# Optimization experiments

Hardware: AMD Instinct MI355X
Metric: run time of the kernel (lower is better)

## Reference

```python
import jax, jax.numpy as jnp
import numpy as np

B, N = 128, 2048
QUERY_DIM, NODE_DIM, OUT_DIM = 256, 128, 256
LAMBDA_INIT = 0.8
LN_EPS = 1e-5


def setup_inputs() -> dict:
    key = jax.random.key(0)
    ks = jax.random.split(key, 8)
    fp_vec = jax.random.normal(ks[0], (B, QUERY_DIM), dtype=jnp.float32)
    node_mat = jax.random.normal(ks[1], (B, N, NODE_DIM), dtype=jnp.float32)
    mask = jax.random.uniform(ks[2], (B, N)) < 0.75
    s = 1.0 / np.sqrt(QUERY_DIM)
    Wq1 = jax.random.uniform(ks[3], (NODE_DIM, QUERY_DIM), minval=-s, maxval=s, dtype=jnp.float32)
    Wq2 = jax.random.uniform(ks[4], (NODE_DIM, QUERY_DIM), minval=-s, maxval=s, dtype=jnp.float32)
    s2 = 1.0 / np.sqrt(NODE_DIM)
    Wk = jax.random.uniform(ks[5], (NODE_DIM, NODE_DIM), minval=-s2, maxval=s2, dtype=jnp.float32)
    Wv = jax.random.uniform(ks[6], (OUT_DIM, NODE_DIM), minval=-s2, maxval=s2, dtype=jnp.float32)
    lambda_logit = jnp.zeros((1,), dtype=jnp.float32)
    gamma = jnp.ones((OUT_DIM,), dtype=jnp.float32)
    beta = jnp.zeros((OUT_DIM,), dtype=jnp.float32)
    return {"fp_vec": fp_vec, "node_mat": node_mat, "mask": mask,
            "Wq1": Wq1, "Wq2": Wq2, "Wk": Wk, "Wv": Wv,
            "lambda_logit": lambda_logit, "gamma": gamma, "beta": beta}


def reference(fp_vec, node_mat, mask, Wq1, Wq2, Wk, Wv, lambda_logit, gamma, beta):
    node_dim = node_mat.shape[-1]
    inv_scale = 1.0 / jnp.sqrt(jnp.asarray(node_dim, jnp.float32))
    # projections (torch Linear: y = x @ W.T)
    q1 = fp_vec @ Wq1.T            # (B, node_dim)
    q2 = fp_vec @ Wq2.T            # (B, node_dim)
    k = jnp.einsum('bnd,ed->bne', node_mat, Wk)   # (B, N, node_dim)
    v = jnp.einsum('bnd,od->bno', node_mat, Wv)   # (B, N, out_dim)
    # single-query scores over nodes
    s1 = jnp.einsum('bd,bnd->bn', q1, k) * inv_scale
    s2 = jnp.einsum('bd,bnd->bn', q2, k) * inv_scale
    pad = jnp.where(mask, 0.0, -1e9).astype(s1.dtype)  # (B, N)
    A1 = jax.nn.softmax(s1 + pad, axis=-1)
    A2 = jax.nn.softmax(s2 + pad, axis=-1)
    lam = LAMBDA_INIT + jax.nn.sigmoid(lambda_logit) * 0.2  # (1,)
    A_diff = A1 - lam * A2         # dropout inactive (eval)
    z = jnp.einsum('bn,bno->bo', A_diff, v)  # (B, out_dim)
    # LayerNorm
    mu = jnp.mean(z, axis=-1, keepdims=True)
    var = jnp.mean(jnp.square(z - mu), axis=-1, keepdims=True)
    return (z - mu) * jax.lax.rsqrt(var + LN_EPS) * gamma + beta
```

## Files before the change

kernel.cpp:

```cpp
#include <hip/hip_runtime.h>
#include <hip/hip_bf16.h>
#include <math.h>

#define BB 128
#define NN 2048
#define ND 128
#define QD 256
#define OD 256

#define NPART 8
#define ROWS_PER_BLOCK (NN / NPART)
#define ROWS_PER_WAVE  (ROWS_PER_BLOCK / 4)
#define STEPS 8
#define STEP_ROWS (ROWS_PER_WAVE / STEPS)
#define STEP_BYTES (STEP_ROWS * ND * 4)
#define PART_STRIDE 260

#define EXP2F(x) __builtin_amdgcn_exp2f(x)

typedef __attribute__((address_space(1))) const void gvoid_t;
typedef __attribute__((address_space(3))) void lvoid_t;

__global__ __launch_bounds__(128) void proj_kernel(
    const float* __restrict__ fp_vec, const float* __restrict__ Wq1,
    const float* __restrict__ Wq2, const float* __restrict__ Wk,
    float* __restrict__ qk1g, float* __restrict__ qk2g)
{
  __shared__ __align__(16) float fp_s[QD];
  __shared__ float q1_s[ND];
  __shared__ float q2_s[ND];
  const int b = blockIdx.x, t = threadIdx.x;
  fp_s[t]       = fp_vec[b * QD + t];
  fp_s[t + 128] = fp_vec[b * QD + 128 + t];
  __syncthreads();
  float a1 = 0.f, a2 = 0.f;
  const float4* w1p = (const float4*)(Wq1 + t * QD);
  const float4* w2p = (const float4*)(Wq2 + t * QD);
  #pragma unroll 8
  for (int q = 0; q < QD / 4; ++q) {
    float4 wa = w1p[q], wb = w2p[q];
    float4 f = *(const float4*)&fp_s[q * 4];
    a1 += f.x * wa.x + f.y * wa.y + f.z * wa.z + f.w * wa.w;
    a2 += f.x * wb.x + f.y * wb.y + f.z * wb.z + f.w * wb.w;
  }
  q1_s[t] = a1;
  q2_s[t] = a2;
  __syncthreads();
  float k1 = 0.f, k2 = 0.f;
  #pragma unroll 8
  for (int e = 0; e < ND; ++e) {
    float wv = Wk[e * ND + t];
    k1 += q1_s[e] * wv;
    k2 += q2_s[e] * wv;
  }
  const float cscale = 0.08838834764831845f * 1.4426950408889634f;
  qk1g[b * ND + t] = k1 * cscale;
  qk2g[b * ND + t] = k2 * cscale;
}

__global__ __launch_bounds__(256, 4) void attn_kernel(
    const float* __restrict__ node, const int* __restrict__ mask,
    const float* __restrict__ qk1g, const float* __restrict__ qk2g,
    float* __restrict__ part)
{
  const int bid = blockIdx.x;
  const int b   = bid >> 3;
  const int oct = bid & (NPART - 1);
  const int t = threadIdx.x;
  const int w = t >> 6;
  const int lane = t & 63;
  const int half = lane >> 5;
  const int hl = lane & 31;

  __shared__ __align__(16) float tile_s[4][2][STEP_ROWS * ND];
  __shared__ __align__(16) float sw1[4][ND], sw2[4][ND];
  __shared__ float sl1[4], sl2[4];

  const int wrow0 = oct * ROWS_PER_BLOCK + w * ROWS_PER_WAVE;

  const float4 qk1 = *(const float4*)(qk1g + b * ND + hl * 4);
  const float4 qk2 = *(const float4*)(qk2g + b * ND + hl * 4);
  const int mv = mask[b * NN + wrow0 + lane];

  const char* gbase = (const char*)node + (size_t)(b * NN + wrow0) * (ND * 4);
  char* lb0 = (char*)&tile_s[w][0][0];
  char* lb1 = (char*)&tile_s[w][1][0];

  #pragma unroll
  for (int i = 0; i < 4; ++i)
    __builtin_amdgcn_global_load_lds(
        (gvoid_t*)(gbase + lane * 16 + i * 1024),
        (lvoid_t*)(lb0 + i * 1024), 16, 0, 0);
  #pragma unroll
  for (int i = 0; i < 4; ++i)
    __builtin_amdgcn_global_load_lds(
        (gvoid_t*)(gbase + STEP_BYTES + lane * 16 + i * 1024),
        (lvoid_t*)(lb1 + i * 1024), 16, 0, 0);

  const float pv = mv ? 0.f : -1e9f;

  float l1 = 0.f, l2 = 0.f;
  float4 w1 = make_float4(0.f, 0.f, 0.f, 0.f);
  float4 w2 = make_float4(0.f, 0.f, 0.f, 0.f);

  #pragma unroll 2
  for (int s = 0; s < STEPS; ++s) {
    if (s < STEPS - 1) asm volatile("s_waitcnt vmcnt(4)" ::: "memory");
    else               asm volatile("s_waitcnt vmcnt(0)" ::: "memory");
    __builtin_amdgcn_sched_barrier(0);

    const float* buf = &tile_s[w][s & 1][0];
    const int ib = s * STEP_ROWS;

    #pragma unroll
    for (int j = 0; j < STEP_ROWS / 2; ++j) {
      const float4 x = *(const float4*)&buf[(2 * j + half) * ND + hl * 4];
      float d1 = x.x * qk1.x + x.y * qk1.y + x.z * qk1.z + x.w * qk1.w;
      float d2 = x.x * qk2.x + x.y * qk2.y + x.z * qk2.z + x.w * qk2.w;
      float e1 = d1 + __shfl_xor(d1, 1, 64);
      float e2 = d2 + __shfl_xor(d2, 1, 64);
      float m = (lane & 1) ? e2 : e1;
      m += __shfl_xor(m, 2, 64);
      m += __shfl_xor(m, 4, 64);
      m += __shfl_xor(m, 8, 64);
      m += __shfl_xor(m, 16, 64);
      const float mo = __shfl_xor(m, 1, 64);
      const float s1 = (lane & 1) ? mo : m;
      const float s2 = (lane & 1) ? m : mo;
      const float pad = __shfl(pv, ib + 2 * j + half, 64);
      const float p1 = EXP2F(s1 + pad);
      const float p2 = EXP2F(s2 + pad);
      l1 += p1;
      l2 += p2;
      w1.x += p1 * x.x; w1.y += p1 * x.y; w1.z += p1 * x.z; w1.w += p1 * x.w;
      w2.x += p2 * x.x; w2.y += p2 * x.y; w2.z += p2 * x.z; w2.w += p2 * x.w;
    }

    asm volatile("s_waitcnt lgkmcnt(0)" ::: "memory");
    if (s + 2 < STEPS) {
      const char* gs = gbase + (size_t)(s + 2) * STEP_BYTES + lane * 16;
      char* ls = (char*)&tile_s[w][s & 1][0];
      #pragma unroll
      for (int i = 0; i < 4; ++i)
        __builtin_amdgcn_global_load_lds(
            (gvoid_t*)(gs + i * 1024),
            (lvoid_t*)(ls + i * 1024), 16, 0, 0);
    }
  }

  l1 += __shfl_xor(l1, 32, 64);
  l2 += __shfl_xor(l2, 32, 64);
  w1.x += __shfl_xor(w1.x, 32, 64); w1.y += __shfl_xor(w1.y, 32, 64);
  w1.z += __shfl_xor(w1.z, 32, 64); w1.w += __shfl_xor(w1.w, 32, 64);
  w2.x += __shfl_xor(w2.x, 32, 64); w2.y += __shfl_xor(w2.y, 32, 64);
  w2.z += __shfl_xor(w2.z, 32, 64); w2.w += __shfl_xor(w2.w, 32, 64);
  if (half == 0) {
    *(float4*)&sw1[w][hl * 4] = w1;
    *(float4*)&sw2[w][hl * 4] = w2;
    if (hl == 0) { sl1[w] = l1; sl2[w] = l2; }
  }
  __syncthreads();

  float* po = part + (size_t)bid * PART_STRIDE;
  if (t == 0) {
    po[0] = sl1[0] + sl1[1] + sl1[2] + sl1[3];
    po[1] = sl2[0] + sl2[1] + sl2[2] + sl2[3];
  }
  if (t < ND) {
    po[4 + t]   = sw1[0][t] + sw1[1][t] + sw1[2][t] + sw1[3][t];
    po[132 + t] = sw2[0][t] + sw2[1][t] + sw2[2][t] + sw2[3][t];
  }
}

__global__ __launch_bounds__(256) void finish_kernel(
    const float* __restrict__ part, const float* __restrict__ Wv,
    const float* __restrict__ lambda_logit, const float* __restrict__ gamma,
    const float* __restrict__ beta, float* __restrict__ out)
{
  const int b = blockIdx.x, t = threadIdx.x;
  __shared__ __align__(16) float wd_s[ND];
  __shared__ float red[8];

  const float lam = 0.8f + 0.2f / (1.f + __expf(-lambda_logit[0]));
  const float* pb = part + (size_t)b * NPART * PART_STRIDE;

  if (t < ND) {
    float L1 = 0.f, L2 = 0.f, W1 = 0.f, W2 = 0.f;
    #pragma unroll
    for (int i = 0; i < NPART; ++i) {
      const float* pc = pb + (size_t)i * PART_STRIDE;
      L1 += pc[0];
      L2 += pc[1];
      W1 += pc[4 + t];
      W2 += pc[132 + t];
    }
    wd_s[t] = W1 / L1 - lam * (W2 / L2);
  }
  __syncthreads();

  float z = 0.f;
  const float4* wvp = (const float4*)(Wv + t * ND);
  #pragma unroll 8
  for (int d = 0; d < ND / 4; ++d) {
    const float4 w = wvp[d];
    const float4 f = *(const float4*)&wd_s[d * 4];
    z += f.x * w.x + f.y * w.y + f.z * w.z + f.w * w.w;
  }

  const int wave = t >> 6, lane = t & 63;
  float s = z;
  #pragma unroll
  for (int off = 32; off; off >>= 1) s += __shfl_xor(s, off, 64);
  if (lane == 0) red[wave] = s;
  __syncthreads();
  const float mu = (red[0] + red[1] + red[2] + red[3]) * (1.f / OD);
  const float dz = z - mu;
  float vs = dz * dz;
  #pragma unroll
  for (int off = 32; off; off >>= 1) vs += __shfl_xor(vs, off, 64);
  if (lane == 0) red[wave + 4] = vs;
  __syncthreads();
  const float var = (red[4] + red[5] + red[6] + red[7]) * (1.f / OD);
  out[b * OD + t] = dz * rsqrtf(var + 1e-5f) * gamma[t] + beta[t];
}

extern "C" void kernel_launch(void* const* d_in, const int* in_sizes, int n_in,
                              void* d_out, int out_size, void* d_ws, size_t ws_size,
                              hipStream_t stream) {
  const float* fp_vec = (const float*)d_in[0];
  const float* node   = (const float*)d_in[1];
  const int*   mask   = (const int*)d_in[2];
  const float* Wq1    = (const float*)d_in[3];
  const float* Wq2    = (const float*)d_in[4];
  const float* Wk     = (const float*)d_in[5];
  const float* Wv     = (const float*)d_in[6];
  const float* ll     = (const float*)d_in[7];
  const float* gamma  = (const float*)d_in[8];
  const float* beta   = (const float*)d_in[9];
  float* out = (float*)d_out;

  float* qk1g = (float*)d_ws;
  float* qk2g = qk1g + BB * ND;
  float* part = qk2g + BB * ND;

  proj_kernel<<<BB, 128, 0, stream>>>(fp_vec, Wq1, Wq2, Wk, qk1g, qk2g);
  attn_kernel<<<BB * NPART, 256, 0, stream>>>(node, mask, qk1g, qk2g, part);
  finish_kernel<<<BB, 256, 0, stream>>>(part, Wv, ll, gamma, beta, out);
}
```

Baseline: 235.7 us.

## Replace LDS double-buffered async loads with direct global loads and more partitions

Removes the per-wave LDS staging pipeline built on global_load_lds with manual vmcnt waits, and has each lane read its float4 node slice straight from global memory in a loop unrolled by 4. The partition count per batch doubles to 16, so there are twice as many blocks, each with 32 rows per wave. The aim is to drop LDS traffic and waitcnt stalls and raise occupancy and parallelism, relying on the compiler's unrolling to keep enough loads in flight. In exchange, latency hiding is no longer explicit, and the finish kernel must reduce twice as many partials.

```diff
diff --git a/kernel.cpp b/kernel.cpp
--- a/kernel.cpp
+++ b/kernel.cpp
@@ -8,18 +8,12 @@
 #define QD 256
 #define OD 256
 
-#define NPART 8
+#define NPART 16
 #define ROWS_PER_BLOCK (NN / NPART)
 #define ROWS_PER_WAVE  (ROWS_PER_BLOCK / 4)
-#define STEPS 8
-#define STEP_ROWS (ROWS_PER_WAVE / STEPS)
-#define STEP_BYTES (STEP_ROWS * ND * 4)
 #define PART_STRIDE 260
 
 #define EXP2F(x) __builtin_amdgcn_exp2f(x)
-
-typedef __attribute__((address_space(1))) const void gvoid_t;
-typedef __attribute__((address_space(3))) void lvoid_t;
 
 __global__ __launch_bounds__(128) void proj_kernel(
     const float* __restrict__ fp_vec, const float* __restrict__ Wq1,
@@ -64,7 +58,7 @@
     float* __restrict__ part)
 {
   const int bid = blockIdx.x;
-  const int b   = bid >> 3;
+  const int b   = bid >> 4;
   const int oct = bid & (NPART - 1);
   const int t = threadIdx.x;
   const int w = t >> 6;
@@ -72,7 +66,6 @@
   const int half = lane >> 5;
   const int hl = lane & 31;
 
-  __shared__ __align__(16) float tile_s[4][2][STEP_ROWS * ND];
   __shared__ __align__(16) float sw1[4][ND], sw2[4][ND];
   __shared__ float sl1[4], sl2[4];
 
@@ -80,72 +73,37 @@
 
   const float4 qk1 = *(const float4*)(qk1g + b * ND + hl * 4);
   const float4 qk2 = *(const float4*)(qk2g + b * ND + hl * 4);
-  const int mv = mask[b * NN + wrow0 + lane];
-
-  const char* gbase = (const char*)node + (size_t)(b * NN + wrow0) * (ND * 4);
-  char* lb0 = (char*)&tile_s[w][0][0];
-  char* lb1 = (char*)&tile_s[w][1][0];
-
-  #pragma unroll
-  for (int i = 0; i < 4; ++i)
-    __builtin_amdgcn_global_load_lds(
-        (gvoid_t*)(gbase + lane * 16 + i * 1024),
-        (lvoid_t*)(lb0 + i * 1024), 16, 0, 0);
-  #pragma unroll
-  for (int i = 0; i < 4; ++i)
-    __builtin_amdgcn_global_load_lds(
-        (gvoid_t*)(gbase + STEP_BYTES + lane * 16 + i * 1024),
-        (lvoid_t*)(lb1 + i * 1024), 16, 0, 0);
-
+  const int mv = mask[b * NN + wrow0 + (lane & 31)];
   const float pv = mv ? 0.f : -1e9f;
+
+  const float* gbase = node + ((size_t)(b * NN + wrow0)) * ND + hl * 4;
 
   float l1 = 0.f, l2 = 0.f;
   float4 w1 = make_float4(0.f, 0.f, 0.f, 0.f);
   float4 w2 = make_float4(0.f, 0.f, 0.f, 0.f);
 
-  #pragma unroll 2
-  for (int s = 0; s < STEPS; ++s) {
-    if (s < STEPS - 1) asm volatile("s_waitcnt vmcnt(4)" ::: "memory");
-    else               asm volatile("s_waitcnt vmcnt(0)" ::: "memory");
-    __builtin_amdgcn_sched_barrier(0);
-
-    const float* buf = &tile_s[w][s & 1][0];
-    const int ib = s * STEP_ROWS;
-
-    #pragma unroll
-    for (int j = 0; j < STEP_ROWS / 2; ++j) {
-      const float4 x = *(const float4*)&buf[(2 * j + half) * ND + hl * 4];
-      float d1 = x.x * qk1.x + x.y * qk1.y + x.z * qk1.z + x.w * qk1.w;
-      float d2 = x.x * qk2.x + x.y * qk2.y + x.z * qk2.z + x.w * qk2.w;
-      float e1 = d1 + __shfl_xor(d1, 1, 64);
-      float e2 = d2 + __shfl_xor(d2, 1, 64);
-      float m = (lane & 1) ? e2 : e1;
-      m += __shfl_xor(m, 2, 64);
-      m += __shfl_xor(m, 4, 64);
-      m += __shfl_xor(m, 8, 64);
-      m += __shfl_xor(m, 16, 64);
-      const float mo = __shfl_xor(m, 1, 64);
-      const float s1 = (lane & 1) ? mo : m;
-      const float s2 = (lane & 1) ? m : mo;
-      const float pad = __shfl(pv, ib + 2 * j + half, 64);
-      const float p1 = EXP2F(s1 + pad);
-      const float p2 = EXP2F(s2 + pad);
-      l1 += p1;
-      l2 += p2;
-      w1.x += p1 * x.x; w1.y += p1 * x.y; w1.z += p1 * x.z; w1.w += p1 * x.w;
-      w2.x += p2 * x.x; w2.y += p2 * x.y; w2.z += p2 * x.z; w2.w += p2 * x.w;
-    }
-
-    asm volatile("s_waitcnt lgkmcnt(0)" ::: "memory");
-    if (s + 2 < STEPS) {
-      const char* gs = gbase + (size_t)(s + 2) * STEP_BYTES + lane * 16;
-      char* ls = (char*)&tile_s[w][s & 1][0];
-      #pragma unroll
-      for (int i = 0; i < 4; ++i)
-        __builtin_amdgcn_global_load_lds(
-            (gvoid_t*)(gs + i * 1024),
-            (lvoid_t*)(ls + i * 1024), 16, 0, 0);
-    }
+  #pragma unroll 4
+  for (int j = 0; j < ROWS_PER_WAVE / 2; ++j) {
+    const float4 x = *(const float4*)(gbase + (size_t)(2 * j + half) * ND);
+    float d1 = x.x * qk1.x + x.y * qk1.y + x.z * qk1.z + x.w * qk1.w;
+    float d2 = x.x * qk2.x + x.y * qk2.y + x.z * qk2.z + x.w * qk2.w;
+    float e1 = d1 + __shfl_xor(d1, 1, 64);
+    float e2 = d2 + __shfl_xor(d2, 1, 64);
+    float m = (lane & 1) ? e2 : e1;
+    m += __shfl_xor(m, 2, 64);
+    m += __shfl_xor(m, 4, 64);
+    m += __shfl_xor(m, 8, 64);
+    m += __shfl_xor(m, 16, 64);
+    const float mo = __shfl_xor(m, 1, 64);
+    const float s1 = (lane & 1) ? mo : m;
+    const float s2 = (lane & 1) ? m : mo;
+    const float pad = __shfl(pv, 2 * j + half, 64);
+    const float p1 = EXP2F(s1 + pad);
+    const float p2 = EXP2F(s2 + pad);
+    l1 += p1;
+    l2 += p2;
+    w1.x += p1 * x.x; w1.y += p1 * x.y; w1.z += p1 * x.z; w1.w += p1 * x.w;
+    w2.x += p2 * x.x; w2.y += p2 * x.y; w2.z += p2 * x.z; w2.w += p2 * x.w;
   }
 
   l1 += __shfl_xor(l1, 32, 64);
```

New measurement: 237.9 us (median of 2 runs). Within noise of the previous version (+0.9%).
